# Kernel optimization log

Hardware: AMD Instinct MI355X
Metric: run time of the kernel (lower is better)

The kernel has to match this reference:

```python
import jax, jax.numpy as jnp
import numpy as np

EPS = 1e-8  # torch CosineSimilarity eps


def _cosine_sim_matrix(x, y):
    # x: [Nx, D], y: [Ny, D] -> [Nx, Ny] cosine similarity via normalized GEMM
    xn = x / jnp.maximum(jnp.linalg.norm(x, axis=-1, keepdims=True), EPS)
    yn = y / jnp.maximum(jnp.linalg.norm(y, axis=-1, keepdims=True), EPS)
    return xn @ yn.T


def setup_inputs() -> dict:
    key = jax.random.key(0)
    k1, k2, k3, k4 = jax.random.split(key, 4)
    N, D, C = 4096, 512, 100
    inst_embed = jax.random.normal(k1, (N, D), dtype=jnp.float32)
    proxy = jax.random.normal(k2, (N, D), dtype=jnp.float32)
    # binary positive-selection mask per class over the batch
    negative_mask = (jax.random.uniform(k3, (C, N)) > 0.5).astype(jnp.float32)
    labels = jax.random.randint(k4, (N,), 0, C, dtype=jnp.int64)
    temperature = jnp.float32(0.1)
    margin = jnp.float32(0.0)
    return {"inst_embed": inst_embed, "proxy": proxy,
            "negative_mask": negative_mask, "labels": labels,
            "temperature": temperature, "margin": margin}


def reference(inst_embed, proxy, negative_mask, labels, temperature, margin):
    # [N, N] similarity matrices
    p2i = _cosine_sim_matrix(proxy, inst_embed)
    i2i = _cosine_sim_matrix(inst_embed, inst_embed)
    p2i_zone = jnp.exp((p2i - margin) / temperature)
    i2i_zone = jnp.exp((i2i - margin) / temperature)
    mask = negative_mask[labels]  # [N, N]
    p2i_num = (p2i_zone * mask).sum(axis=1)
    i2i_num = (i2i_zone * mask).sum(axis=1)
    p2i_den = p2i_zone.sum(axis=1)
    i2i_den = i2i_zone.sum(axis=1)
    p2i_loss = -jnp.log(temperature * (p2i_num / p2i_den)).mean()
    i2i_loss = -jnp.log(temperature * (i2i_num / i2i_den)).mean()
    return p2i_loss + i2i_loss
```

## Files before the change

### kernel.cpp

```cpp
#include <hip/hip_runtime.h>
#include <hip/hip_bf16.h>

#define D_DIM 512
#define KSTEPS 16
#define BM 64
#define BN 64
#define GRIDY 8

typedef __bf16 bf16x8 __attribute__((ext_vector_type(8)));
typedef float  f32x4  __attribute__((ext_vector_type(4)));

__device__ __forceinline__ unsigned short f2bf_rne(float x) {
    unsigned int u = __float_as_uint(x);
    u += 0x7FFFu + ((u >> 16) & 1u);
    return (unsigned short)(u >> 16);
}

__device__ __forceinline__ void g2l16(const void* g, void* l) {
    __builtin_amdgcn_global_load_lds(
        (const __attribute__((address_space(1))) unsigned int*)g,
        (__attribute__((address_space(3))) unsigned int*)l, 16, 0, 0);
}

__global__ __launch_bounds__(128) void normalize_rows(
    const float* __restrict__ inst, const float* __restrict__ proxy,
    unsigned short* __restrict__ instb, unsigned short* __restrict__ proxyb, int N)
{
    int row = blockIdx.x;
    const float* src;
    unsigned short* dst;
    if (row < N) { src = inst  + (size_t)row * D_DIM;        dst = instb  + (size_t)row * D_DIM; }
    else         { src = proxy + (size_t)(row - N) * D_DIM;  dst = proxyb + (size_t)(row - N) * D_DIM; }
    int t = threadIdx.x;
    float4 v = ((const float4*)src)[t];
    float ss = v.x*v.x + v.y*v.y + v.z*v.z + v.w*v.w;
    #pragma unroll
    for (int off = 32; off > 0; off >>= 1) ss += __shfl_down(ss, off, 64);
    __shared__ float wss[2];
    if ((t & 63) == 0) wss[t >> 6] = ss;
    __syncthreads();
    float inv = 1.0f / fmaxf(sqrtf(wss[0] + wss[1]), 1e-8f);
    ushort4 o;
    o.x = f2bf_rne(v.x * inv); o.y = f2bf_rne(v.y * inv);
    o.z = f2bf_rne(v.z * inv); o.w = f2bf_rne(v.w * inv);
    ((ushort4*)dst)[t] = o;
}

__global__ __launch_bounds__(256, 2) void fused_scores(
    const unsigned short* __restrict__ instb,
    const unsigned short* __restrict__ proxyb,
    const float* __restrict__ negmask,
    const int*  __restrict__ labels,
    const float* __restrict__ temp_p,
    const float* __restrict__ margin_p,
    float* __restrict__ nd,
    int N, int colsPerBlock)
{
    __shared__ unsigned short Bt[BN * D_DIM];

    const int tid  = threadIdx.x;
    const int lane = tid & 63;
    const int wave = tid >> 6;
    const int quad = lane >> 4;
    const int l16  = lane & 15;

    const int row0 = blockIdx.x * BM + wave * 16;

    const float temp  = *temp_p;
    const float scale = 1.44269504088896340736f / temp;
    const float bias  = -(*margin_p) * scale;

    bf16x8 Ap[KSTEPS], Ai[KSTEPS];
    {
        const unsigned short* pr = proxyb + (size_t)(row0 + l16) * D_DIM + quad * 8;
        const unsigned short* ir = instb  + (size_t)(row0 + l16) * D_DIM + quad * 8;
        #pragma unroll
        for (int ks = 0; ks < KSTEPS; ks++) {
            Ap[ks] = *(const bf16x8*)(pr + ks * 32);
            Ai[ks] = *(const bf16x8*)(ir + ks * 32);
        }
    }

    int lab[4];
    #pragma unroll
    for (int r = 0; r < 4; r++) lab[r] = labels[row0 + quad * 4 + r];

    float numP[4] = {0.f,0.f,0.f,0.f}, denP[4] = {0.f,0.f,0.f,0.f};
    float numI[4] = {0.f,0.f,0.f,0.f}, denI[4] = {0.f,0.f,0.f,0.f};

    const int j0base = blockIdx.y * colsPerBlock;
    for (int jt = 0; jt < colsPerBlock; jt += BN) {
        const int j0 = j0base + jt;
        __syncthreads();
        #pragma unroll
        for (int it = 0; it < (BN * (D_DIM / 8)) / 256; it++) {
            const int br = it * 4 + wave;
            const unsigned short* src =
                instb + (size_t)(j0 + br) * D_DIM + ((lane ^ (br & 7)) * 8);
            g2l16(src, &Bt[(size_t)(it * 256 + wave * 64) * 8]);
        }
        __syncthreads();

        f32x4 accP[4] = {}, accI[4] = {};
        #pragma unroll
        for (int ks = 0; ks < KSTEPS; ks++) {
            #pragma unroll
            for (int cg = 0; cg < 4; cg++) {
                const int rB  = cg * 16 + l16;
                const int chs = (ks * 4 + quad) ^ (rB & 7);
                bf16x8 b = *(const bf16x8*)&Bt[(size_t)rB * D_DIM + chs * 8];
                accP[cg] = __builtin_amdgcn_mfma_f32_16x16x32_bf16(Ap[ks], b, accP[cg], 0, 0, 0);
                accI[cg] = __builtin_amdgcn_mfma_f32_16x16x32_bf16(Ai[ks], b, accI[cg], 0, 0, 0);
            }
        }

        #pragma unroll
        for (int cg = 0; cg < 4; cg++) {
            const int j = j0 + cg * 16 + l16;
            #pragma unroll
            for (int r = 0; r < 4; r++) {
                const float m = negmask[(size_t)lab[r] * N + j];
                float zp = exp2f(accP[cg][r] * scale + bias);
                float zi = exp2f(accI[cg][r] * scale + bias);
                denP[r] += zp; numP[r] += zp * m;
                denI[r] += zi; numI[r] += zi * m;
            }
        }
    }

    #pragma unroll
    for (int r = 0; r < 4; r++) {
        float np = numP[r], dp = denP[r], ni = numI[r], di = denI[r];
        #pragma unroll
        for (int off = 8; off > 0; off >>= 1) {
            np += __shfl_down(np, off, 16);
            dp += __shfl_down(dp, off, 16);
            ni += __shfl_down(ni, off, 16);
            di += __shfl_down(di, off, 16);
        }
        if (l16 == 0) {
            const int row = row0 + quad * 4 + r;
            atomicAdd(&nd[row],         np);
            atomicAdd(&nd[N + row],     dp);
            atomicAdd(&nd[2 * N + row], ni);
            atomicAdd(&nd[3 * N + row], di);
        }
    }
}

__global__ __launch_bounds__(1024) void loss_reduce(
    const float* __restrict__ nd, const float* __restrict__ temp_p,
    float* __restrict__ out, int N)
{
    const float t = *temp_p;
    float s = 0.f;
    for (int i = threadIdx.x; i < N; i += 1024) {
        s += (logf(nd[N + i])     - logf(nd[i]));
        s += (logf(nd[3 * N + i]) - logf(nd[2 * N + i]));
    }
    #pragma unroll
    for (int off = 32; off > 0; off >>= 1) s += __shfl_down(s, off, 64);
    __shared__ float wss[16];
    if ((threadIdx.x & 63) == 0) wss[threadIdx.x >> 6] = s;
    __syncthreads();
    if (threadIdx.x < 16) {
        float v = wss[threadIdx.x];
        #pragma unroll
        for (int off = 8; off > 0; off >>= 1) v += __shfl_down(v, off, 16);
        if (threadIdx.x == 0) out[0] = v / (float)N - 2.0f * logf(t);
    }
}

extern "C" void kernel_launch(void* const* d_in, const int* in_sizes, int n_in,
                              void* d_out, int out_size, void* d_ws, size_t ws_size,
                              hipStream_t stream)
{
    const float* inst     = (const float*)d_in[0];
    const float* proxy    = (const float*)d_in[1];
    const float* negmask  = (const float*)d_in[2];
    const int*   labels   = (const int*)d_in[3];
    const float* temp_p   = (const float*)d_in[4];
    const float* margin_p = (const float*)d_in[5];
    float* out = (float*)d_out;

    const int N = in_sizes[3];

    unsigned short* instb  = (unsigned short*)d_ws;
    unsigned short* proxyb = instb + (size_t)N * D_DIM;
    float* nd = (float*)(proxyb + (size_t)N * D_DIM);

    hipMemsetAsync(nd, 0, sizeof(float) * 4 * N, stream);
    normalize_rows<<<2 * N, 128, 0, stream>>>(inst, proxy, instb, proxyb, N);
    dim3 grid(N / BM, GRIDY);
    fused_scores<<<grid, 256, 0, stream>>>(instb, proxyb, negmask, labels,
                                           temp_p, margin_p, nd, N, N / GRIDY);
    loss_reduce<<<1, 1024, 0, stream>>>(nd, temp_p, out, N);
}
```

Before: 121.4 us.

## Double-buffer B tiles in LDS and fold memset into normalize kernel

The score kernel now double-buffers half-size (32-column) B tiles in LDS, so the async global-to-LDS load of the next tile overlaps with MFMA compute on the current one. The normalize kernel processes 4 rows per wave with 256-thread blocks and butterfly shuffles instead of shared memory. It also zeroes the accumulator buffer, which removes the separate memset launch. The trade-off is smaller tiles with more loop iterations, and correctness depends on the async LDS loads completing before the barrier that follows them.

After: 119.9 us. About the same (-1.2%).

```diff
diff --git a/kernel.cpp b/kernel.cpp
--- a/kernel.cpp
+++ b/kernel.cpp
@@ -4,7 +4,7 @@
 #define D_DIM 512
 #define KSTEPS 16
 #define BM 64
-#define BN 64
+#define BN 32
 #define GRIDY 8
 
 typedef __bf16 bf16x8 __attribute__((ext_vector_type(8)));
@@ -22,28 +22,38 @@
         (__attribute__((address_space(3))) unsigned int*)l, 16, 0, 0);
 }
 
-__global__ __launch_bounds__(128) void normalize_rows(
+__global__ __launch_bounds__(256) void normalize_rows(
     const float* __restrict__ inst, const float* __restrict__ proxy,
-    unsigned short* __restrict__ instb, unsigned short* __restrict__ proxyb, int N)
-{
-    int row = blockIdx.x;
-    const float* src;
-    unsigned short* dst;
-    if (row < N) { src = inst  + (size_t)row * D_DIM;        dst = instb  + (size_t)row * D_DIM; }
-    else         { src = proxy + (size_t)(row - N) * D_DIM;  dst = proxyb + (size_t)(row - N) * D_DIM; }
-    int t = threadIdx.x;
-    float4 v = ((const float4*)src)[t];
-    float ss = v.x*v.x + v.y*v.y + v.z*v.z + v.w*v.w;
-    #pragma unroll
-    for (int off = 32; off > 0; off >>= 1) ss += __shfl_down(ss, off, 64);
-    __shared__ float wss[2];
-    if ((t & 63) == 0) wss[t >> 6] = ss;
-    __syncthreads();
-    float inv = 1.0f / fmaxf(sqrtf(wss[0] + wss[1]), 1e-8f);
-    ushort4 o;
-    o.x = f2bf_rne(v.x * inv); o.y = f2bf_rne(v.y * inv);
-    o.z = f2bf_rne(v.z * inv); o.w = f2bf_rne(v.w * inv);
-    ((ushort4*)dst)[t] = o;
+    unsigned short* __restrict__ instb, unsigned short* __restrict__ proxyb,
+    float* __restrict__ nd, int N)
+{
+    const int lane = threadIdx.x & 63;
+    const int wave = threadIdx.x >> 6;
+    const int base = blockIdx.x * 16 + wave * 4;
+    #pragma unroll
+    for (int i = 0; i < 4; ++i) {
+        const int row = base + i;
+        const float* src;
+        unsigned short* dst;
+        if (row < N) { src = inst  + (size_t)row * D_DIM;        dst = instb  + (size_t)row * D_DIM; }
+        else         { src = proxy + (size_t)(row - N) * D_DIM;  dst = proxyb + (size_t)(row - N) * D_DIM; }
+        float4 v0 = ((const float4*)src)[lane * 2];
+        float4 v1 = ((const float4*)src)[lane * 2 + 1];
+        float ss = v0.x*v0.x + v0.y*v0.y + v0.z*v0.z + v0.w*v0.w
+                 + v1.x*v1.x + v1.y*v1.y + v1.z*v1.z + v1.w*v1.w;
+        #pragma unroll
+        for (int off = 32; off > 0; off >>= 1) ss += __shfl_xor(ss, off, 64);
+        const float inv = 1.0f / fmaxf(sqrtf(ss), 1e-8f);
+        ushort4 o0, o1;
+        o0.x = f2bf_rne(v0.x * inv); o0.y = f2bf_rne(v0.y * inv);
+        o0.z = f2bf_rne(v0.z * inv); o0.w = f2bf_rne(v0.w * inv);
+        o1.x = f2bf_rne(v1.x * inv); o1.y = f2bf_rne(v1.y * inv);
+        o1.z = f2bf_rne(v1.z * inv); o1.w = f2bf_rne(v1.w * inv);
+        ((ushort4*)dst)[lane * 2]     = o0;
+        ((ushort4*)dst)[lane * 2 + 1] = o1;
+    }
+    if (blockIdx.x < 16)
+        ((float4*)nd)[blockIdx.x * 256 + threadIdx.x] = make_float4(0.f, 0.f, 0.f, 0.f);
 }
 
 __global__ __launch_bounds__(256, 2) void fused_scores(
@@ -56,7 +66,8 @@
     float* __restrict__ nd,
     int N, int colsPerBlock)
 {
-    __shared__ unsigned short Bt[BN * D_DIM];
+    __shared__ unsigned short Bt0[BN * D_DIM];
+    __shared__ unsigned short Bt1[BN * D_DIM];
 
     const int tid  = threadIdx.x;
     const int lane = tid & 63;
@@ -89,36 +100,38 @@
     float numI[4] = {0.f,0.f,0.f,0.f}, denI[4] = {0.f,0.f,0.f,0.f};
 
     const int j0base = blockIdx.y * colsPerBlock;
-    for (int jt = 0; jt < colsPerBlock; jt += BN) {
-        const int j0 = j0base + jt;
-        __syncthreads();
-        #pragma unroll
-        for (int it = 0; it < (BN * (D_DIM / 8)) / 256; it++) {
+    const int nt     = colsPerBlock / BN;
+
+    auto stage = [&](unsigned short (&B)[BN * D_DIM], int t) {
+        const int j0 = j0base + t * BN;
+        #pragma unroll
+        for (int it = 0; it < BN / 4; ++it) {
             const int br = it * 4 + wave;
             const unsigned short* src =
                 instb + (size_t)(j0 + br) * D_DIM + ((lane ^ (br & 7)) * 8);
-            g2l16(src, &Bt[(size_t)(it * 256 + wave * 64) * 8]);
-        }
-        __syncthreads();
-
-        f32x4 accP[4] = {}, accI[4] = {};
-        #pragma unroll
-        for (int ks = 0; ks < KSTEPS; ks++) {
+            g2l16(src, &B[br * D_DIM]);
+        }
+    };
+
+    auto compute = [&](unsigned short (&B)[BN * D_DIM], int t) {
+        const int j0 = j0base + t * BN;
+        f32x4 accP[2] = {}, accI[2] = {};
+        #pragma unroll
+        for (int ks = 0; ks < KSTEPS; ++ks) {
             #pragma unroll
-            for (int cg = 0; cg < 4; cg++) {
+            for (int cg = 0; cg < 2; ++cg) {
                 const int rB  = cg * 16 + l16;
                 const int chs = (ks * 4 + quad) ^ (rB & 7);
-                bf16x8 b = *(const bf16x8*)&Bt[(size_t)rB * D_DIM + chs * 8];
+                bf16x8 b = *(const bf16x8*)&B[(size_t)rB * D_DIM + chs * 8];
                 accP[cg] = __builtin_amdgcn_mfma_f32_16x16x32_bf16(Ap[ks], b, accP[cg], 0, 0, 0);
                 accI[cg] = __builtin_amdgcn_mfma_f32_16x16x32_bf16(Ai[ks], b, accI[cg], 0, 0, 0);
             }
         }
-
-        #pragma unroll
-        for (int cg = 0; cg < 4; cg++) {
+        #pragma unroll
+        for (int cg = 0; cg < 2; ++cg) {
             const int j = j0 + cg * 16 + l16;
             #pragma unroll
-            for (int r = 0; r < 4; r++) {
+            for (int r = 0; r < 4; ++r) {
                 const float m = negmask[(size_t)lab[r] * N + j];
                 float zp = exp2f(accP[cg][r] * scale + bias);
                 float zi = exp2f(accI[cg][r] * scale + bias);
@@ -126,6 +139,17 @@
                 denI[r] += zi; numI[r] += zi * m;
             }
         }
+    };
+
+    stage(Bt0, 0);
+    __syncthreads();
+    for (int t = 0; t < nt; t += 2) {
+        stage(Bt1, t + 1);
+        compute(Bt0, t);
+        __syncthreads();
+        if (t + 2 < nt) stage(Bt0, t + 2);
+        compute(Bt1, t + 1);
+        __syncthreads();
     }
 
     #pragma unroll
@@ -189,8 +213,7 @@
     unsigned short* proxyb = instb + (size_t)N * D_DIM;
     float* nd = (float*)(proxyb + (size_t)N * D_DIM);
 
-    hipMemsetAsync(nd, 0, sizeof(float) * 4 * N, stream);
-    normalize_rows<<<2 * N, 128, 0, stream>>>(inst, proxy, instb, proxyb, N);
+    normalize_rows<<<2 * N / 16, 256, 0, stream>>>(inst, proxy, instb, proxyb, nd, N);
     dim3 grid(N / BM, GRIDY);
     fused_scores<<<grid, 256, 0, stream>>>(instb, proxyb, negmask, labels,
                                            temp_p, margin_p, nd, N, N / GRIDY);
```
